# Kernel tuning notes

Measured on AMD Instinct MI355X. Metric: run time of the kernel, lower is better.

Reference implementation:

```python
import jax, jax.numpy as jnp
import numpy as np

B, S, D, H, L, FFN = 32, 512, 512, 8, 4, 1024
DH = D // H
EPS = 1e-5


def make_pe(seq, d):
    pos = np.arange(seq)[:, None].astype(np.float64)
    i = np.arange(d)[None, :]
    angle = pos / np.power(10000.0, (i // 2 * 2.0) / d)
    pe = angle.copy()
    pe[:, 0::2] = np.sin(angle[:, 0::2])
    pe[:, 1::2] = np.cos(angle[:, 1::2])
    return jnp.asarray(pe, dtype=jnp.float32)


def layer_norm(x, g, b):
    mu = jnp.mean(x, axis=-1, keepdims=True)
    var = jnp.mean((x - mu) ** 2, axis=-1, keepdims=True)
    return (x - mu) * jax.lax.rsqrt(var + EPS) * g + b


def setup_inputs() -> dict:
    key = jax.random.key(0)
    ks = jax.random.split(key, 12)
    sd = 0.02
    d = {
        "x": jax.random.normal(ks[0], (B, S, D), dtype=jnp.float32),
        "pe": make_pe(S, D),
        "Wq": jax.random.normal(ks[1], (L, D, D), dtype=jnp.float32) * sd,
        "bq": jnp.zeros((L, D), dtype=jnp.float32),
        "Wk": jax.random.normal(ks[2], (L, D, D), dtype=jnp.float32) * sd,
        "bk": jnp.zeros((L, D), dtype=jnp.float32),
        "Wv": jax.random.normal(ks[3], (L, D, D), dtype=jnp.float32) * sd,
        "bv": jnp.zeros((L, D), dtype=jnp.float32),
        "Wo": jax.random.normal(ks[4], (L, D, D), dtype=jnp.float32) * sd,
        "bo": jnp.zeros((L, D), dtype=jnp.float32),
        "ln1_g": jnp.ones((L, D), dtype=jnp.float32),
        "ln1_b": jnp.zeros((L, D), dtype=jnp.float32),
        "W1": jax.random.normal(ks[5], (L, D, FFN), dtype=jnp.float32) * sd,
        "b1": jnp.zeros((L, FFN), dtype=jnp.float32),
        "W2": jax.random.normal(ks[6], (L, FFN, D), dtype=jnp.float32) * sd,
        "b2": jnp.zeros((L, D), dtype=jnp.float32),
        "ln2_g": jnp.ones((L, D), dtype=jnp.float32),
        "ln2_b": jnp.zeros((L, D), dtype=jnp.float32),
    }
    return d


def reference(x, pe, Wq, bq, Wk, bk, Wv, bv, Wo, bo, ln1_g, ln1_b,
              W1, b1, W2, b2, ln2_g, ln2_b):
    out = x + pe  # positional encoding (dropout = identity in eval)
    scale = DH ** (-0.5)
    for l in range(L):
        # projections (B,S,D)
        Q = out @ Wq[l] + bq[l]
        K = out @ Wk[l] + bk[l]
        V = out @ Wv[l] + bv[l]
        # faithful raw view (no head transpose), matching torch .view semantics
        Qh = Q.reshape(B * H, S, DH)
        Kh = K.reshape(B * H, S, DH)
        Vh = V.reshape(B * H, S, DH)
        att = jnp.einsum('bqd,bkd->bqk', Qh, Kh) * scale  # (B*H,S,S)
        att = jax.nn.softmax(att, axis=-1)
        ctx = jnp.einsum('bqk,bkd->bqd', att, Vh).reshape(B, S, D)
        a = layer_norm(ctx @ Wo[l] + bo[l] + out, ln1_g[l], ln1_b[l])
        # position-wise FFN
        h = jax.nn.relu(a @ W1[l] + b1[l])
        out = layer_norm(h @ W2[l] + b2[l] + a, ln2_g[l], ln2_b[l])
    return out.reshape(B, S * D)
```

## Files before the change

kernel.cpp:

```cpp
#include <hip/hip_runtime.h>
#include <stdint.h>

#define NB 32
#define NS 512
#define ND 512
#define NH 8
#define NL 4
#define NF 1024
#define NDH 64
#define NM (NB*NS)
#define WLSTRIDE 2097152
#define CSCALE 0.18033688f

typedef __attribute__((ext_vector_type(8))) short bf16x8;
typedef __attribute__((ext_vector_type(4))) short s16x4;
typedef __attribute__((ext_vector_type(4))) float f32x4;
typedef __attribute__((ext_vector_type(2))) uint32_t u32x2;

#define VM0  asm volatile("s_waitcnt vmcnt(0)" ::: "memory")
#define VM4  asm volatile("s_waitcnt vmcnt(4)" ::: "memory")
#define VM8  asm volatile("s_waitcnt vmcnt(8)" ::: "memory")
#define SCHB __builtin_amdgcn_sched_barrier(0)
#define SB   __builtin_amdgcn_s_barrier()

__device__ __forceinline__ short f2bf(float f) {
    union { float f; uint32_t u; } v; v.f = f;
    uint32_t r = (v.u + 0x7FFFu + ((v.u >> 16) & 1u)) >> 16;
    return (short)r;
}
__device__ __forceinline__ float bf2f(short s) {
    union { uint32_t u; float f; } v; v.u = ((uint32_t)(uint16_t)s) << 16;
    return v.f;
}
__device__ __forceinline__ f32x4 mfma16(bf16x8 a, bf16x8 b, f32x4 c) {
    return __builtin_amdgcn_mfma_f32_16x16x32_bf16(a, b, c, 0, 0, 0);
}
__device__ __forceinline__ void gld16(const void* g, void* l) {
    __builtin_amdgcn_global_load_lds(
        (const __attribute__((address_space(1))) void*)g,
        (__attribute__((address_space(3))) void*)l, 16, 0, 0);
}
__device__ __forceinline__ uint32_t cvtpk(float a, float b) {
    uint32_t w;
    asm("v_cvt_pk_bf16_f32 %0, %1, %2" : "=v"(w) : "v"(a), "v"(b));
    return w;
}
__device__ __forceinline__ void xcd_swz(int& bx, int& by, int gx, int gy) {
    int n = gx * gy;
    int f = by * gx + bx;
    int q = n >> 3;
    int xcd = f & 7, idx = f >> 3;
    int s = xcd * q + idx;
    bx = s % gx; by = s / gx;
}

__global__ __launch_bounds__(256) void convT_k(const float* __restrict__ src,
        short* __restrict__ dst, int K, int N, int woff)
{
    __shared__ float T[64][65];
    int tk = K >> 6, tn = N >> 6;
    int bid = blockIdx.x;
    int l = bid / (tk * tn), rb = bid % (tk * tn);
    int k0 = (rb / tn) << 6, n0 = (rb % tn) << 6;
    const float* s = src + (size_t)l * K * N;
    short* d = dst + (size_t)l * WLSTRIDE + woff;
    int tr = threadIdx.x >> 4, tc = threadIdx.x & 15;
    #pragma unroll
    for (int p = 0; p < 4; p++) {
        int row = p * 16 + tr;
        f32x4 v = *(const f32x4*)(s + (size_t)(k0 + row) * N + n0 + tc * 4);
        #pragma unroll
        for (int j = 0; j < 4; j++) T[row][tc * 4 + j] = v[j];
    }
    __syncthreads();
    #pragma unroll
    for (int p = 0; p < 4; p++) {
        int nrow = p * 16 + tr;
        s16x4 w;
        #pragma unroll
        for (int j = 0; j < 4; j++) w[j] = f2bf(T[tc * 4 + j][nrow]);
        *(s16x4*)(d + (size_t)(n0 + nrow) * K + k0 + tc * 4) = w;
    }
}

__global__ __launch_bounds__(256) void biaspack_k(const float* __restrict__ bq,
        const float* __restrict__ bk, const float* __restrict__ bv, float* __restrict__ out)
{
    int i = blockIdx.x * 256 + threadIdx.x;
    if (i >= NL * 1536) return;
    int l = i / 1536, j = i - l * 1536;
    float v = (j < 512) ? bq[l * 512 + j] * CSCALE
            : (j < 1024) ? bk[l * 512 + j - 512] : bv[l * 512 + j - 1024];
    out[i] = v;
}

__global__ __launch_bounds__(256) void addpe_k(const float* __restrict__ x,
        const float* __restrict__ pe, short* __restrict__ X)
{
    size_t i = ((size_t)blockIdx.x * 256 + threadIdx.x) * 8;
    size_t sd = i % (size_t)(NS * ND);
    f32x4 a0 = *(const f32x4*)(x + i);
    f32x4 a1 = *(const f32x4*)(x + i + 4);
    f32x4 p0 = *(const f32x4*)(pe + sd);
    f32x4 p1 = *(const f32x4*)(pe + sd + 4);
    bf16x8 r;
    #pragma unroll
    for (int j = 0; j < 4; j++) { r[j] = f2bf(a0[j] + p0[j]); r[4 + j] = f2bf(a1[j] + p1[j]); }
    *(bf16x8*)(X + i) = r;
}

template<int EPI>
__global__ __launch_bounds__(256) void gemm_bt(
        const short* __restrict__ A, const short* __restrict__ Bt,
        const float* __restrict__ bias, const short* __restrict__ res,
        void* __restrict__ C0, void* __restrict__ C1, void* __restrict__ C2,
        int M, int N, int K)
{
    __shared__ __align__(16) short Al[16384];
    __shared__ __align__(16) short Bl[16384];
    const int tid = threadIdx.x;
    const int wid = tid >> 6, lane = tid & 63;
    int bx = blockIdx.x, by = blockIdx.y;
    xcd_swz(bx, by, gridDim.x, gridDim.y);
    const int m0 = by * 128, n0 = bx * 128;
    const int wr = wid >> 1, wc = wid & 1;

    f32x4 acc[4][4];
    f32x4 zz = {0.f, 0.f, 0.f, 0.f};
    #pragma unroll
    for (int i = 0; i < 4; i++)
        #pragma unroll
        for (int j = 0; j < 4; j++) acc[i][j] = zz;

    const size_t rk = (size_t)K * 2;
    const char* Ab = (const char*)A + (size_t)m0 * rk;
    const char* Bb = (const char*)Bt + (size_t)n0 * rk;

    int srow[4], scol[4];
    #pragma unroll
    for (int c = 0; c < 4; c++) {
        int p = c * 4096 + tid * 16;
        int l = p ^ (((p >> 7) & 7) << 4);
        srow[c] = l >> 7;  scol[c] = l & 127;
    }

    auto stage = [&](int dofs, int kt) {
        size_t kb = (size_t)(kt << 6) * 2;
        #pragma unroll
        for (int c = 0; c < 4; c++)
            gld16(Ab + (size_t)srow[c] * rk + kb + scol[c],
                  (char*)Al + dofs + c * 4096 + wid * 1024);
        #pragma unroll
        for (int c = 0; c < 4; c++)
            gld16(Bb + (size_t)srow[c] * rk + kb + scol[c],
                  (char*)Bl + dofs + c * 4096 + wid * 1024);
    };
    auto compute = [&](int dofs) {
        #pragma unroll
        for (int ks = 0; ks < 2; ks++) {
            bf16x8 af[4], bfr[4];
            #pragma unroll
            for (int mf = 0; mf < 4; mf++) {
                int row = wr * 64 + mf * 16 + (lane & 15);
                int off = (row * 128 + ks * 64 + ((lane >> 4) * 16)) ^ ((row & 7) << 4);
                af[mf] = *(const bf16x8*)((const char*)Al + dofs + off);
            }
            #pragma unroll
            for (int nf = 0; nf < 4; nf++) {
                int row = wc * 64 + nf * 16 + (lane & 15);
                int off = (row * 128 + ks * 64 + ((lane >> 4) * 16)) ^ ((row & 7) << 4);
                bfr[nf] = *(const bf16x8*)((const char*)Bl + dofs + off);
            }
            #pragma unroll
            for (int mf = 0; mf < 4; mf++)
                #pragma unroll
                for (int nf = 0; nf < 4; nf++)
                    acc[mf][nf] = mfma16(af[mf], bfr[nf], acc[mf][nf]);
        }
    };

    const int nt = K >> 6;
    stage(0, 0);
    stage(16384, 1);
    VM8; SCHB; SB;
    for (int t = 0; t < nt; t += 2) {
        compute(0);
        SB;
        if (t + 2 < nt) { stage(0, t + 2); VM8; } else VM0;
        SCHB; SB;
        compute(16384);
        SB;
        if (t + 3 < nt) { stage(16384, t + 3); VM8; } else VM0;
        SCHB; SB;
    }

    int seg = 0;
    void* outp;
    int colbase, ostride;
    if (EPI == 0) {
        seg = n0 >> 9;
        outp = (seg == 0) ? C0 : (seg == 1) ? C1 : C2;
        colbase = n0 & 511; ostride = 512;
    } else {
        outp = C0; colbase = n0; ostride = N;
    }

    #pragma unroll
    for (int mf = 0; mf < 4; mf++) {
        #pragma unroll
        for (int nf = 0; nf < 4; nf++) {
            int colg = n0 + wc * 64 + nf * 16 + (lane & 15);
            int col  = colbase + wc * 64 + nf * 16 + (lane & 15);
            float bi = bias[colg];
            #pragma unroll
            for (int r = 0; r < 4; r++) {
                int row = m0 + wr * 64 + mf * 16 + ((lane >> 4) << 2) + r;
                float v;
                if (EPI == 0 && seg == 0) v = acc[mf][nf][r] * CSCALE + bi;
                else                      v = acc[mf][nf][r] + bi;
                if (EPI == 0) {
                    ((short*)outp)[(size_t)row * 512 + col] = f2bf(v);
                } else if (EPI == 1) {
                    ((short*)outp)[(size_t)row * ostride + col] = f2bf(fmaxf(v, 0.f));
                } else {
                    v += bf2f(res[(size_t)row * ostride + col]);
                    ((float*)outp)[(size_t)row * ostride + col] = v;
                }
            }
        }
    }
}

__global__ __launch_bounds__(256) void vtrans_k(const short* __restrict__ V,
        short* __restrict__ VT)
{
    __shared__ short T[64][65];
    const int tid = threadIdx.x;
    const int r0 = blockIdx.x * 64, g = blockIdx.y;
    const size_t base = (size_t)g * 32768;
    #pragma unroll
    for (int rep = 0; rep < 2; rep++) {
        int chunk = rep * 256 + tid;
        int sr = chunk >> 3, c8 = (chunk & 7) * 8;
        bf16x8 v = *(const bf16x8*)(V + base + (size_t)(r0 + sr) * 64 + c8);
        #pragma unroll
        for (int j = 0; j < 8; j++) T[sr][c8 + j] = v[j];
    }
    __syncthreads();
    #pragma unroll
    for (int rep = 0; rep < 2; rep++) {
        int chunk = rep * 256 + tid;
        int dh = chunk >> 3, c8 = (chunk & 7) * 8;
        bf16x8 w;
        #pragma unroll
        for (int j = 0; j < 8; j++) w[j] = T[c8 + j][dh];
        *(bf16x8*)(VT + base + (size_t)dh * 512 + r0 + c8) = w;
    }
}

__global__ __launch_bounds__(256) void attn_k(
        const short* __restrict__ Q, const short* __restrict__ Kb,
        const short* __restrict__ VT, short* __restrict__ ctx)
{
    __shared__ __align__(16) short Kl[8192];
    __shared__ __align__(16) short Vl[8192];
    __shared__ __align__(16) short Pl[8192];
    const int tid = threadIdx.x, wid = tid >> 6, lane = tid & 63;
    int bx = blockIdx.x, by = blockIdx.y;
    xcd_swz(bx, by, gridDim.x, gridDim.y);
    const int g = by, q0 = bx * 128;
    const size_t base = (size_t)g * 32768;

    bf16x8 qa[2][2];
    #pragma unroll
    for (int qf = 0; qf < 2; qf++)
        #pragma unroll
        for (int ks = 0; ks < 2; ks++)
            qa[qf][ks] = *(const bf16x8*)(Q + base
                + (size_t)(q0 + wid * 32 + qf * 16 + (lane & 15)) * 64
                + ks * 32 + ((lane >> 4) * 8));

    f32x4 o[2][4];
    float ps[2][4];
    f32x4 zz = {0.f, 0.f, 0.f, 0.f};
    #pragma unroll
    for (int qf = 0; qf < 2; qf++) {
        #pragma unroll
        for (int nf = 0; nf < 4; nf++) o[qf][nf] = zz;
        #pragma unroll
        for (int r = 0; r < 4; r++) ps[qf][r] = 0.f;
    }

    const char* Kbase = (const char*)(Kb + base);
    const char* Vbase = (const char*)(VT + base);

    int ksp[2], srow[2], scol[2];
    #pragma unroll
    for (int c = 0; c < 2; c++) {
        int p = c * 4096 + tid * 16;
        ksp[c] = p ^ (((p >> 9) & 7) << 4);
        int pv = p ^ (((p >> 7) & 7) << 4);
        srow[c] = pv >> 7;  scol[c] = pv & 127;
    }

    auto stage = [&](int dofs, int kt) {
        #pragma unroll
        for (int c = 0; c < 2; c++)
            gld16(Kbase + (size_t)kt * 8192 + ksp[c],
                  (char*)Kl + dofs + c * 4096 + wid * 1024);
        #pragma unroll
        for (int c = 0; c < 2; c++)
            gld16(Vbase + (size_t)srow[c] * 1024 + kt * 128 + scol[c],
                  (char*)Vl + dofs + c * 4096 + wid * 1024);
    };

    auto tile = [&](int dofs) {
        f32x4 sc[2][4];
        #pragma unroll
        for (int qf = 0; qf < 2; qf++)
            #pragma unroll
            for (int nf = 0; nf < 4; nf++) sc[qf][nf] = zz;
        #pragma unroll
        for (int ks = 0; ks < 2; ks++) {
            #pragma unroll
            for (int nf = 0; nf < 4; nf++) {
                int kvr = (lane & 15) * 4 + nf;
                int bo = (kvr * 128 + ((ks * 64 + ((lane >> 4) * 16)) ^ (((kvr >> 2) & 7) << 4)))
                         + dofs;
                bf16x8 kf = *(const bf16x8*)((const char*)Kl + bo);
                #pragma unroll
                for (int qf = 0; qf < 2; qf++)
                    sc[qf][nf] = mfma16(qa[qf][ks], kf, sc[qf][nf]);
            }
        }

        #pragma unroll
        for (int qf = 0; qf < 2; qf++) {
            #pragma unroll
            for (int r = 0; r < 4; r++) {
                int qr = wid * 32 + qf * 16 + ((lane >> 4) << 2) + r;
                float e0 = __builtin_amdgcn_exp2f(sc[qf][0][r]);
                float e1 = __builtin_amdgcn_exp2f(sc[qf][1][r]);
                float e2 = __builtin_amdgcn_exp2f(sc[qf][2][r]);
                float e3 = __builtin_amdgcn_exp2f(sc[qf][3][r]);
                ps[qf][r] += (e0 + e1) + (e2 + e3);
                u32x2 w;
                w[0] = cvtpk(e0, e1);
                w[1] = cvtpk(e2, e3);
                int bo = (qr * 128 + (lane & 15) * 8) ^ ((qr & 7) << 4);
                *(u32x2*)((char*)Pl + bo) = w;
            }
        }

        #pragma unroll
        for (int ks = 0; ks < 2; ks++) {
            bf16x8 pa[2];
            #pragma unroll
            for (int qf = 0; qf < 2; qf++) {
                int qrb = wid * 32 + qf * 16 + (lane & 15);
                int bo = (qrb * 128 + ks * 64 + ((lane >> 4) * 16)) ^ ((qrb & 7) << 4);
                pa[qf] = *(const bf16x8*)((const char*)Pl + bo);
            }
            #pragma unroll
            for (int nf = 0; nf < 4; nf++) {
                int dh = nf * 16 + (lane & 15);
                int bo2 = ((dh * 128 + ks * 64 + ((lane >> 4) * 16)) ^ ((dh & 7) << 4)) + dofs;
                bf16x8 vf = *(const bf16x8*)((const char*)Vl + bo2);
                #pragma unroll
                for (int qf = 0; qf < 2; qf++)
                    o[qf][nf] = mfma16(pa[qf], vf, o[qf][nf]);
            }
        }
    };

    stage(0, 0);
    stage(8192, 1);
    VM4; SCHB; SB;
    for (int kt = 0; kt < 8; kt += 2) {
        tile(0);
        SB;
        if (kt + 2 < 8) { stage(0, kt + 2); VM4; } else VM0;
        SCHB; SB;
        tile(8192);
        SB;
        if (kt + 3 < 8) { stage(8192, kt + 3); VM4; } else VM0;
        SCHB; SB;
    }

    #pragma unroll
    for (int qf = 0; qf < 2; qf++) {
        #pragma unroll
        for (int r = 0; r < 4; r++) {
            float s = ps[qf][r];
            s += __shfl_xor(s, 1);
            s += __shfl_xor(s, 2);
            s += __shfl_xor(s, 4);
            s += __shfl_xor(s, 8);
            float inv = 1.f / s;
            int qr = q0 + wid * 32 + qf * 16 + ((lane >> 4) << 2) + r;
            #pragma unroll
            for (int nf = 0; nf < 4; nf++) {
                int dh = nf * 16 + (lane & 15);
                ctx[base + (size_t)qr * 64 + dh] = f2bf(o[qf][nf][r] * inv);
            }
        }
    }
}

template<int OUTF32>
__global__ __launch_bounds__(256) void ln_k(
        const float* __restrict__ pre, const float* __restrict__ g,
        const float* __restrict__ b, void* __restrict__ out)
{
    int row = blockIdx.x * 4 + (threadIdx.x >> 6);
    int lane = threadIdx.x & 63;
    const float* x = pre + (size_t)row * ND + lane * 8;
    f32x4 a0 = *(const f32x4*)x;
    f32x4 a1 = *(const f32x4*)(x + 4);
    float s = 0.f, sq = 0.f;
    #pragma unroll
    for (int j = 0; j < 4; j++) { s += a0[j]; sq += a0[j] * a0[j]; s += a1[j]; sq += a1[j] * a1[j]; }
    #pragma unroll
    for (int d = 1; d < 64; d <<= 1) { s += __shfl_xor(s, d); sq += __shfl_xor(sq, d); }
    float mean = s * (1.f / ND);
    float var = sq * (1.f / ND) - mean * mean;
    float rstd = rsqrtf(var + 1e-5f);
    const float* gp = g + lane * 8;
    const float* bp = b + lane * 8;
    if (OUTF32) {
        float* op = (float*)out + (size_t)row * ND + lane * 8;
        f32x4 r0, r1;
        #pragma unroll
        for (int j = 0; j < 4; j++) {
            r0[j] = (a0[j] - mean) * rstd * gp[j] + bp[j];
            r1[j] = (a1[j] - mean) * rstd * gp[4 + j] + bp[4 + j];
        }
        *(f32x4*)op = r0;
        *(f32x4*)(op + 4) = r1;
    } else {
        bf16x8 rr;
        #pragma unroll
        for (int j = 0; j < 4; j++) {
            rr[j]     = f2bf((a0[j] - mean) * rstd * gp[j] + bp[j]);
            rr[4 + j] = f2bf((a1[j] - mean) * rstd * gp[4 + j] + bp[4 + j]);
        }
        *(bf16x8*)((short*)out + (size_t)row * ND + lane * 8) = rr;
    }
}

extern "C" void kernel_launch(void* const* d_in, const int* in_sizes, int n_in,
                              void* d_out, int out_size, void* d_ws, size_t ws_size,
                              hipStream_t stream)
{
    (void)in_sizes; (void)n_in; (void)out_size; (void)ws_size;
    const float* x   = (const float*)d_in[0];
    const float* pe  = (const float*)d_in[1];
    const float* Wq  = (const float*)d_in[2];
    const float* bq  = (const float*)d_in[3];
    const float* Wk  = (const float*)d_in[4];
    const float* bk  = (const float*)d_in[5];
    const float* Wv  = (const float*)d_in[6];
    const float* bv  = (const float*)d_in[7];
    const float* Wo  = (const float*)d_in[8];
    const float* bo  = (const float*)d_in[9];
    const float* g1  = (const float*)d_in[10];
    const float* be1 = (const float*)d_in[11];
    const float* W1  = (const float*)d_in[12];
    const float* b1  = (const float*)d_in[13];
    const float* W2  = (const float*)d_in[14];
    const float* b2  = (const float*)d_in[15];
    const float* g2  = (const float*)d_in[16];
    const float* be2 = (const float*)d_in[17];

    char* ws = (char*)d_ws;
    const size_t MB = 1048576;
    short* WT   = (short*)(ws);
    short* XB   = (short*)(ws + 16 * MB);
    short* QB   = (short*)(ws + 32 * MB);
    short* KB   = (short*)(ws + 48 * MB);
    short* VB   = (short*)(ws + 64 * MB);
    short* VTb  = (short*)(ws + 80 * MB);
    short* CT   = (short*)(ws + 96 * MB);
    float* BQKV = (float*)(ws + 112 * MB);
    short* AB   = QB;
    float* PR   = (float*)KB;
    short* HB   = VTb;

    convT_k<<<dim3(NL*8*8),  256, 0, stream>>>(Wq, WT, ND, ND, 0);
    convT_k<<<dim3(NL*8*8),  256, 0, stream>>>(Wk, WT, ND, ND, 262144);
    convT_k<<<dim3(NL*8*8),  256, 0, stream>>>(Wv, WT, ND, ND, 524288);
    convT_k<<<dim3(NL*8*8),  256, 0, stream>>>(Wo, WT, ND, ND, 786432);
    convT_k<<<dim3(NL*8*16), 256, 0, stream>>>(W1, WT, ND, NF, 1048576);
    convT_k<<<dim3(NL*16*8), 256, 0, stream>>>(W2, WT, NF, ND, 1572864);
    biaspack_k<<<dim3(24), 256, 0, stream>>>(bq, bk, bv, BQKV);

    addpe_k<<<dim3(4096), 256, 0, stream>>>(x, pe, XB);

    for (int l = 0; l < NL; l++) {
        const short* wl = WT + (size_t)l * WLSTRIDE;
        gemm_bt<0><<<dim3(12, 128), 256, 0, stream>>>(XB, wl, BQKV + l*1536, nullptr,
                                                      QB, KB, VB, NM, 1536, ND);
        vtrans_k<<<dim3(8, 256), 256, 0, stream>>>(VB, VTb);
        attn_k<<<dim3(4, 256), 256, 0, stream>>>(QB, KB, VTb, CT);
        gemm_bt<2><<<dim3(4, 128), 256, 0, stream>>>(CT, wl + 786432, bo + l*ND, XB,
                                                     PR, nullptr, nullptr, NM, ND, ND);
        ln_k<0><<<dim3(4096), 256, 0, stream>>>(PR, g1 + l*ND, be1 + l*ND, AB);
        gemm_bt<1><<<dim3(8, 128), 256, 0, stream>>>(AB, wl + 1048576, b1 + l*NF, nullptr,
                                                     HB, nullptr, nullptr, NM, NF, ND);
        gemm_bt<2><<<dim3(4, 128), 256, 0, stream>>>(HB, wl + 1572864, b2 + l*ND, AB,
                                                     PR, nullptr, nullptr, NM, ND, NF);
        if (l < NL - 1)
            ln_k<0><<<dim3(4096), 256, 0, stream>>>(PR, g2 + l*ND, be2 + l*ND, XB);
        else
            ln_k<1><<<dim3(4096), 256, 0, stream>>>(PR, g2 + l*ND, be2 + l*ND, (float*)d_out);
    }
}
```

Measured before the change: 760.0 us.

## Permute B-operand column mapping so epilogue stores four contiguous columns

The GEMM B tile and the attention V tile are now loaded with a row swizzle keyed on groups of four rows. Each lane's MFMA column fragments then map to four consecutive output columns (lane*4+nf) instead of columns strided by 16. This lets the GEMM epilogue, and the attention context write, use a vector bias load, packed bf16 stores and vector residual loads and float4 stores in place of scalar per-element accesses. It changes the LDS addressing pattern for B and V reads, which could introduce bank conflicts if the new swizzle is not conflict-free.

Measured after the change: 761.1 us. No clear change (+0.2%).

```diff
diff --git a/kernel.cpp b/kernel.cpp
--- a/kernel.cpp
+++ b/kernel.cpp
@@ -136,23 +136,25 @@
     const char* Ab = (const char*)A + (size_t)m0 * rk;
     const char* Bb = (const char*)Bt + (size_t)n0 * rk;
 
-    int srow[4], scol[4];
+    int srA[4], scA[4], srB[4], scB[4];
     #pragma unroll
     for (int c = 0; c < 4; c++) {
         int p = c * 4096 + tid * 16;
-        int l = p ^ (((p >> 7) & 7) << 4);
-        srow[c] = l >> 7;  scol[c] = l & 127;
+        int la = p ^ (((p >> 7) & 7) << 4);
+        srA[c] = la >> 7;  scA[c] = la & 127;
+        int lb = p ^ (((p >> 9) & 7) << 4);
+        srB[c] = lb >> 7;  scB[c] = lb & 127;
     }
 
     auto stage = [&](int dofs, int kt) {
         size_t kb = (size_t)(kt << 6) * 2;
         #pragma unroll
         for (int c = 0; c < 4; c++)
-            gld16(Ab + (size_t)srow[c] * rk + kb + scol[c],
+            gld16(Ab + (size_t)srA[c] * rk + kb + scA[c],
                   (char*)Al + dofs + c * 4096 + wid * 1024);
         #pragma unroll
         for (int c = 0; c < 4; c++)
-            gld16(Bb + (size_t)srow[c] * rk + kb + scol[c],
+            gld16(Bb + (size_t)srB[c] * rk + kb + scB[c],
                   (char*)Bl + dofs + c * 4096 + wid * 1024);
     };
     auto compute = [&](int dofs) {
@@ -167,8 +169,9 @@
             }
             #pragma unroll
             for (int nf = 0; nf < 4; nf++) {
-                int row = wc * 64 + nf * 16 + (lane & 15);
-                int off = (row * 128 + ks * 64 + ((lane >> 4) * 16)) ^ ((row & 7) << 4);
+                int row = wc * 64 + ((lane & 15) << 2) + nf;
+                int off = row * 128
+                        + ((ks * 64 + ((lane >> 4) * 16)) ^ (((row >> 2) & 7) << 4));
                 bfr[nf] = *(const bf16x8*)((const char*)Bl + dofs + off);
             }
             #pragma unroll
@@ -205,27 +208,33 @@
         outp = C0; colbase = n0; ostride = N;
     }
 
+    const int c0 = wc * 64 + ((lane & 15) << 2);
+    f32x4 bi4 = *(const f32x4*)(bias + n0 + c0);
     #pragma unroll
     for (int mf = 0; mf < 4; mf++) {
         #pragma unroll
-        for (int nf = 0; nf < 4; nf++) {
-            int colg = n0 + wc * 64 + nf * 16 + (lane & 15);
-            int col  = colbase + wc * 64 + nf * 16 + (lane & 15);
-            float bi = bias[colg];
-            #pragma unroll
-            for (int r = 0; r < 4; r++) {
-                int row = m0 + wr * 64 + mf * 16 + ((lane >> 4) << 2) + r;
-                float v;
-                if (EPI == 0 && seg == 0) v = acc[mf][nf][r] * CSCALE + bi;
-                else                      v = acc[mf][nf][r] + bi;
-                if (EPI == 0) {
-                    ((short*)outp)[(size_t)row * 512 + col] = f2bf(v);
-                } else if (EPI == 1) {
-                    ((short*)outp)[(size_t)row * ostride + col] = f2bf(fmaxf(v, 0.f));
-                } else {
-                    v += bf2f(res[(size_t)row * ostride + col]);
-                    ((float*)outp)[(size_t)row * ostride + col] = v;
-                }
+        for (int r = 0; r < 4; r++) {
+            int row = m0 + wr * 64 + mf * 16 + ((lane >> 4) << 2) + r;
+            float v[4];
+            #pragma unroll
+            for (int j = 0; j < 4; j++) {
+                if (EPI == 0 && seg == 0) v[j] = fmaf(acc[mf][j][r], CSCALE, bi4[j]);
+                else                      v[j] = acc[mf][j][r] + bi4[j];
+            }
+            if (EPI == 0) {
+                u32x2 w; w[0] = cvtpk(v[0], v[1]); w[1] = cvtpk(v[2], v[3]);
+                *(u32x2*)((short*)outp + (size_t)row * 512 + colbase + c0) = w;
+            } else if (EPI == 1) {
+                u32x2 w;
+                w[0] = cvtpk(fmaxf(v[0], 0.f), fmaxf(v[1], 0.f));
+                w[1] = cvtpk(fmaxf(v[2], 0.f), fmaxf(v[3], 0.f));
+                *(u32x2*)((short*)outp + (size_t)row * ostride + colbase + c0) = w;
+            } else {
+                s16x4 rr = *(const s16x4*)(res + (size_t)row * ostride + colbase + c0);
+                f32x4 o4;
+                #pragma unroll
+                for (int j = 0; j < 4; j++) o4[j] = v[j] + bf2f(rr[j]);
+                *(f32x4*)((float*)outp + (size_t)row * ostride + colbase + c0) = o4;
             }
         }
     }
@@ -299,8 +308,7 @@
     for (int c = 0; c < 2; c++) {
         int p = c * 4096 + tid * 16;
         ksp[c] = p ^ (((p >> 9) & 7) << 4);
-        int pv = p ^ (((p >> 7) & 7) << 4);
-        srow[c] = pv >> 7;  scol[c] = pv & 127;
+        srow[c] = ksp[c] >> 7;  scol[c] = ksp[c] & 127;
     }
 
     auto stage = [&](int dofs, int kt) {
@@ -324,9 +332,9 @@
         for (int ks = 0; ks < 2; ks++) {
             #pragma unroll
             for (int nf = 0; nf < 4; nf++) {
-                int kvr = (lane & 15) * 4 + nf;
-                int bo = (kvr * 128 + ((ks * 64 + ((lane >> 4) * 16)) ^ (((kvr >> 2) & 7) << 4)))
-                         + dofs;
+                int kvr = ((lane & 15) << 2) + nf;
+                int bo = kvr * 128
+                       + ((ks * 64 + ((lane >> 4) * 16)) ^ (((kvr >> 2) & 7) << 4)) + dofs;
                 bf16x8 kf = *(const bf16x8*)((const char*)Kl + bo);
                 #pragma unroll
                 for (int qf = 0; qf < 2; qf++)
@@ -363,8 +371,9 @@
             }
             #pragma unroll
             for (int nf = 0; nf < 4; nf++) {
-                int dh = nf * 16 + (lane & 15);
-                int bo2 = ((dh * 128 + ks * 64 + ((lane >> 4) * 16)) ^ ((dh & 7) << 4)) + dofs;
+                int dh = ((lane & 15) << 2) + nf;
+                int bo2 = dh * 128
+                        + ((ks * 64 + ((lane >> 4) * 16)) ^ (((dh >> 2) & 7) << 4)) + dofs;
                 bf16x8 vf = *(const bf16x8*)((const char*)Vl + bo2);
                 #pragma unroll
                 for (int qf = 0; qf < 2; qf++)
@@ -398,11 +407,10 @@
             s += __shfl_xor(s, 8);
             float inv = 1.f / s;
             int qr = q0 + wid * 32 + qf * 16 + ((lane >> 4) << 2) + r;
-            #pragma unroll
-            for (int nf = 0; nf < 4; nf++) {
-                int dh = nf * 16 + (lane & 15);
-                ctx[base + (size_t)qr * 64 + dh] = f2bf(o[qf][nf][r] * inv);
-            }
+            u32x2 w;
+            w[0] = cvtpk(o[qf][0][r] * inv, o[qf][1][r] * inv);
+            w[1] = cvtpk(o[qf][2][r] * inv, o[qf][3][r] * inv);
+            *(u32x2*)(ctx + base + (size_t)qr * 64 + ((lane & 15) << 2)) = w;
         }
     }
 }
```
